# Kernel optimization log

Measured on AMD Instinct MI355X. Metric: run time of the kernel, lower is better.

The kernel has to match this reference:

```python
import jax, jax.numpy as jnp
from jax import lax
import numpy as np

EPS = 0.15      # constraint_value_upper_bound (per-row box |y/c - 1| <= EPS)
DELTA = 0.05    # groups_constraint_upper_bound (per-group mean |y/c - 1| <= DELTA)
N_GROUPS = 8
N_ITERS = 300   # Dykstra iterations; converges to the exact QP projection

N, D, H1, H2, K = 65536, 512, 1024, 512, 1


def setup_inputs() -> dict:
    key = jax.random.key(0)
    ks = jax.random.split(key, 8)
    x = jax.random.normal(ks[0], (N, D), jnp.float32)
    W1 = jax.random.normal(ks[1], (D, H1), jnp.float32) / np.float32(np.sqrt(D))
    b1 = jnp.zeros((H1,), jnp.float32)
    W2 = jax.random.normal(ks[2], (H1, H2), jnp.float32) / np.float32(np.sqrt(H1))
    b2 = jnp.zeros((H2,), jnp.float32)
    Wf = jax.random.normal(ks[3], (H2, K), jnp.float32) / np.float32(np.sqrt(H2))
    bf = jnp.zeros((K,), jnp.float32)
    c = jax.random.uniform(ks[4], (N,), jnp.float32, 0.5, 2.0)
    # quantiles_price_tensor: q_i = (1/N) * #{k : c_k <= c_i}  (rank via searchsorted)
    q = jnp.searchsorted(jnp.sort(c), c, side='right').astype(jnp.float32) / N
    # group j covers q in [j/G, (j+1)/G]; assign boundary ties to the lower group
    g = jnp.clip(jnp.ceil(q * N_GROUPS).astype(jnp.int32) - 1, 0, N_GROUPS - 1)
    group_mask = jax.nn.one_hot(g, N_GROUPS, dtype=jnp.float32).T  # [G, N]
    return dict(x=x, W1=W1, b1=b1, W2=W2, b2=b2, Wf=Wf, bf=bf,
                constraint_constant=c, group_mask=group_mask)


def _project(y_u, c, group_mask):
    """Exact QP: min ||y - y_u||^2 s.t. |y_i/c_i - 1| <= EPS and
    |mean_{i in G_j}(y_i/c_i - 1)| <= DELTA, solved by Dykstra's alternating
    projections in z = y/c - 1 space under the weighted norm sum c_i^2 z_i^2."""
    w = c * c                                   # [N] weights of the norm
    z0 = y_u / c[:, None] - 1.0                 # [N, K]
    n = group_mask.sum(axis=1)                  # [G] group sizes
    a = group_mask / n[:, None]                 # [G, N] averaging rows
    denom = (a * a / w[None, :]).sum(axis=1)    # [G]  a^T W^{-1} a
    u = (a / w[None, :]) / denom[:, None]       # [G, N] weighted slab directions

    def proj_box(z):
        return jnp.clip(z, -EPS, EPS)

    def proj_grp(z):
        v = a @ z                               # [G, K] group means
        return z - u.T @ (v - jnp.clip(v, -DELTA, DELTA))

    def body(carry, _):
        z, p, q = carry
        zb = proj_box(z + p); p = z + p - zb
        zg = proj_grp(zb + q); q = zb + q - zg
        return (zg, p, q), None

    init = (z0, jnp.zeros_like(z0), jnp.zeros_like(z0))
    (z, _, _), _ = lax.scan(body, init, None, length=N_ITERS)
    return (z + 1.0) * c[:, None]


def reference(x, W1, b1, W2, b2, Wf, bf, constraint_constant, group_mask):
    h = jax.nn.relu(x @ W1 + b1)   # Dropout is identity in eval mode
    h = jax.nn.relu(h @ W2 + b2)
    y_u = h @ Wf + bf              # [N, 1] unconstrained predictions
    return _project(y_u, constraint_constant, group_mask)
```

## Files before the change

### kernel.cpp

```cpp
#include <hip/hip_runtime.h>
#include <hip/hip_bf16.h>

#define NROWS 65536
#define DIM   512
#define H1DIM 1024
#define H2DIM 512
#define EPSC  0.15f
#define DELTA 0.05f
#define NGRP  8
#define CAPG  16384

typedef __bf16 bf16x8 __attribute__((ext_vector_type(8)));
typedef float  f32x4  __attribute__((ext_vector_type(4)));

__device__ __forceinline__ void gload16(const void* g, void* lds) {
  __builtin_amdgcn_global_load_lds((__attribute__((address_space(1))) const unsigned int*)g,
                                   (__attribute__((address_space(3))) unsigned int*)lds,
                                   16, 0, 0);
}

__global__ void k_zero(float* y_u, int n, int* cnt) {
  int i = blockIdx.x * blockDim.x + threadIdx.x;
  if (i < n) y_u[i] = 0.f;
  if (i < NGRP) cnt[i] = 0;
}

__global__ void k_tcvt(const float* __restrict__ src, __bf16* __restrict__ dst, int R, int C) {
  __shared__ float tile[32][33];
  const int bi = blockIdx.x * 32;
  const int bj = blockIdx.y * 32;
  const int tx = threadIdx.x, ty = threadIdx.y;
  #pragma unroll
  for (int r = ty; r < 32; r += 8)
    tile[r][tx] = src[(size_t)(bi + r) * C + bj + tx];
  __syncthreads();
  #pragma unroll
  for (int r = ty; r < 32; r += 8)
    dst[(size_t)(bj + r) * R + bi + tx] = (__bf16)tile[tx][r];
}

__global__ __launch_bounds__(512, 2) void k_gemm1(const float* __restrict__ x,
                                                  const __bf16* __restrict__ w1t,
                                                  const float* __restrict__ b1,
                                                  __bf16* __restrict__ h1, int row0) {
  __shared__ __align__(16) __bf16 As[2][256 * 64];
  __shared__ __align__(16) __bf16 Bs[2][256 * 64];
  const int tid = threadIdx.x;
  const int w = tid >> 6, l = tid & 63;
  const int mt   = (int)gridDim.x >> 2;
  const int mper = mt >> 3;
  const int xcd  = blockIdx.x & 7;
  const int idx  = blockIdx.x >> 3;
  const int brow = (xcd * mper + (idx >> 2)) * 256;
  const int bcol = (idx & 3) * 256;
  const int lr = l & 15, lk = l >> 4;
  const int wm = w >> 2, wn = w & 3;
  const int mbase = wm * 128, nbase = wn * 64;
  const int srow = w * 32 + (l >> 3);
  const int scol = (l & 7) * 8;
  const int NT = DIM / 64;
  f32x4 acc[8][4] = {};
  const float* xp = x + (size_t)(row0 + brow + srow) * DIM + scol;

  #define LOADA(KT, F) do { \
    _Pragma("unroll") for (int t_ = 0; t_ < 4; ++t_) { \
      const float* s_ = xp + (size_t)(t_ * 8) * DIM + (KT); \
      F[t_][0] = *(const float4*)s_; F[t_][1] = *(const float4*)(s_ + 4); } } while (0)
  #define STOREB(KT, BUF) do { \
    _Pragma("unroll") for (int t_ = 0; t_ < 4; ++t_) \
      gload16(w1t + (size_t)(bcol + srow + t_ * 8) * DIM + (KT) + scol, \
              Bs[BUF] + (w * 32 + t_ * 8) * 64); } while (0)
  #define CVTA(BUF, F) do { \
    _Pragma("unroll") for (int t_ = 0; t_ < 4; ++t_) { \
      bf16x8 v_; \
      v_[0] = (__bf16)F[t_][0].x; v_[1] = (__bf16)F[t_][0].y; \
      v_[2] = (__bf16)F[t_][0].z; v_[3] = (__bf16)F[t_][0].w; \
      v_[4] = (__bf16)F[t_][1].x; v_[5] = (__bf16)F[t_][1].y; \
      v_[6] = (__bf16)F[t_][1].z; v_[7] = (__bf16)F[t_][1].w; \
      *(bf16x8*)(As[BUF] + (w * 32 + t_ * 8) * 64 + (l >> 3) * 64 + scol) = v_; } } while (0)
  #define COMPUTE(BUF) do { \
    _Pragma("unroll") for (int kk = 0; kk < 64; kk += 32) { \
      bf16x8 af[8], bq[4]; \
      _Pragma("unroll") for (int m = 0; m < 8; ++m) \
        af[m] = *(const bf16x8*)(As[BUF] + (mbase + m * 16 + lr) * 64 + kk + lk * 8); \
      _Pragma("unroll") for (int nn = 0; nn < 4; ++nn) \
        bq[nn] = *(const bf16x8*)(Bs[BUF] + (nbase + nn * 16 + lr) * 64 + kk + lk * 8); \
      __builtin_amdgcn_s_setprio(1); \
      _Pragma("unroll") for (int m = 0; m < 8; ++m) \
        _Pragma("unroll") for (int nn = 0; nn < 4; ++nn) \
          acc[m][nn] = __builtin_amdgcn_mfma_f32_16x16x32_bf16(af[m], bq[nn], acc[m][nn], 0, 0, 0); \
      __builtin_amdgcn_s_setprio(0); \
    } } while (0)

  {
    float4 f[4][2];
    LOADA(0, f);
    STOREB(0, 0);
    CVTA(0, f);
  }
  __syncthreads();
  int cur = 0;
  for (int t = 0; t < NT - 1; ++t) {
    const int ktn = (t + 1) * 64;
    float4 f[4][2];
    LOADA(ktn, f);
    STOREB(ktn, cur ^ 1);
    COMPUTE(cur);
    CVTA(cur ^ 1, f);
    __syncthreads();
    cur ^= 1;
  }
  COMPUTE(cur);

  #undef LOADA
  #undef STOREB
  #undef CVTA
  #undef COMPUTE

  #pragma unroll
  for (int nn = 0; nn < 4; ++nn) {
    const int col = bcol + nbase + nn * 16 + lr;
    const float bias = b1[col];
    #pragma unroll
    for (int m = 0; m < 8; ++m) {
      const int row = brow + mbase + m * 16 + lk * 4;
      #pragma unroll
      for (int j = 0; j < 4; ++j) {
        float v = acc[m][nn][j] + bias;
        v = fmaxf(v, 0.f);
        h1[(size_t)(row + j) * H1DIM + col] = (__bf16)v;
      }
    }
  }
}

__global__ __launch_bounds__(512, 2) void k_gemm2(const __bf16* __restrict__ h1,
                                                  const __bf16* __restrict__ w2t,
                                                  const float* __restrict__ b2,
                                                  const float* __restrict__ wf,
                                                  float* __restrict__ y_u, int row0) {
  __shared__ __align__(16) __bf16 As[2][256 * 64];
  __shared__ __align__(16) __bf16 Bs[2][256 * 64];
  __shared__ float yred[256];
  const int tid = threadIdx.x;
  const int w = tid >> 6, l = tid & 63;
  const int mt   = (int)gridDim.x >> 1;
  const int mper = mt >> 3;
  const int xcd  = blockIdx.x & 7;
  const int idx  = blockIdx.x >> 3;
  const int brow = (xcd * mper + (idx >> 1)) * 256;
  const int n0   = (idx & 1) * 256;
  const int lr = l & 15, lk = l >> 4;
  const int wm = w >> 2, wn = w & 3;
  const int mbase = wm * 128, nbase = wn * 64;
  const int srow = w * 32 + (l >> 3);
  const int scol = (l & 7) * 8;
  const int NT = H1DIM / 64;
  f32x4 acc[8][4] = {};

  #define STAGE2(KT, BUF) do { \
    _Pragma("unroll") for (int t_ = 0; t_ < 4; ++t_) { \
      gload16(h1  + (size_t)(brow + srow + t_ * 8) * H1DIM + (KT) + scol, \
              As[BUF] + (w * 32 + t_ * 8) * 64); \
      gload16(w2t + (size_t)(n0   + srow + t_ * 8) * H1DIM + (KT) + scol, \
              Bs[BUF] + (w * 32 + t_ * 8) * 64); } } while (0)
  #define COMPUTE2(BUF) do { \
    _Pragma("unroll") for (int kk = 0; kk < 64; kk += 32) { \
      bf16x8 af[8], bq[4]; \
      _Pragma("unroll") for (int m = 0; m < 8; ++m) \
        af[m] = *(const bf16x8*)(As[BUF] + (mbase + m * 16 + lr) * 64 + kk + lk * 8); \
      _Pragma("unroll") for (int nn = 0; nn < 4; ++nn) \
        bq[nn] = *(const bf16x8*)(Bs[BUF] + (nbase + nn * 16 + lr) * 64 + kk + lk * 8); \
      __builtin_amdgcn_s_setprio(1); \
      _Pragma("unroll") for (int m = 0; m < 8; ++m) \
        _Pragma("unroll") for (int nn = 0; nn < 4; ++nn) \
          acc[m][nn] = __builtin_amdgcn_mfma_f32_16x16x32_bf16(af[m], bq[nn], acc[m][nn], 0, 0, 0); \
      __builtin_amdgcn_s_setprio(0); \
    } } while (0)

  STAGE2(0, 0);
  __syncthreads();
  int cur = 0;
  for (int t = 0; t < NT - 1; ++t) {
    STAGE2((t + 1) * 64, cur ^ 1);
    COMPUTE2(cur);
    __syncthreads();
    cur ^= 1;
  }
  COMPUTE2(cur);

  #undef STAGE2
  #undef COMPUTE2

  float yacc[8][4] = {};
  #pragma unroll
  for (int nn = 0; nn < 4; ++nn) {
    const int col = n0 + nbase + nn * 16 + lr;
    const float bias = b2[col];
    const float wfv = wf[col];
    #pragma unroll
    for (int m = 0; m < 8; ++m)
      #pragma unroll
      for (int j = 0; j < 4; ++j)
        yacc[m][j] += fmaxf(acc[m][nn][j] + bias, 0.f) * wfv;
  }
  #pragma unroll
  for (int m = 0; m < 8; ++m)
    #pragma unroll
    for (int j = 0; j < 4; ++j) {
      float v = yacc[m][j];
      v += __shfl_xor(v, 1, 64);
      v += __shfl_xor(v, 2, 64);
      v += __shfl_xor(v, 4, 64);
      v += __shfl_xor(v, 8, 64);
      yacc[m][j] = v;
    }
  if (tid < 256) yred[tid] = 0.f;
  __syncthreads();
  if (lr == 0) {
    #pragma unroll
    for (int m = 0; m < 8; ++m)
      #pragma unroll
      for (int j = 0; j < 4; ++j)
        atomicAdd(&yred[mbase + m * 16 + lk * 4 + j], yacc[m][j]);
  }
  __syncthreads();
  if (tid < 256) atomicAdd(&y_u[row0 + brow + tid], yred[tid]);
}

__global__ __launch_bounds__(256) void k_scatter(const float* __restrict__ y_u,
                                                 const float* __restrict__ c,
                                                 const float* __restrict__ mask,
                                                 const float* __restrict__ bfp,
                                                 float* __restrict__ z0c, float* __restrict__ wc,
                                                 unsigned char* __restrict__ gidx,
                                                 int* __restrict__ cnt, int n) {
  __shared__ int lcnt[NGRP];
  __shared__ int lbase[NGRP];
  const float bf0 = bfp[0];
  const int tid = threadIdx.x;
  if (tid < NGRP) lcnt[tid] = 0;
  __syncthreads();
  const int i = blockIdx.x * blockDim.x + tid;
  int g = 0, slot_l = 0;
  float z0 = 0.f, wv = 0.f;
  if (i < n) {
    const float cv = c[i];
    z0 = (y_u[i] + bf0) / cv - 1.f;
    wv = cv * cv;
    #pragma unroll
    for (int j = 1; j < NGRP; ++j)
      if (mask[(size_t)j * NROWS + i] > 0.5f) g = j;
    slot_l = atomicAdd(&lcnt[g], 1);
    gidx[i] = (unsigned char)g;
  }
  __syncthreads();
  if (tid < NGRP) lbase[tid] = atomicAdd(&cnt[tid], lcnt[tid]);
  __syncthreads();
  if (i < n) {
    const int slot = lbase[g] + slot_l;
    if (slot < CAPG) {
      z0c[(size_t)g * CAPG + slot] = z0;
      wc [(size_t)g * CAPG + slot] = wv;
    }
  }
}

__device__ __forceinline__ float wave_red(float v, int mode) {
  #pragma unroll
  for (int o = 32; o > 0; o >>= 1) {
    float u = __shfl_xor(v, o, 64);
    v = (mode == 0) ? (v + u) : ((mode == 1) ? fmaxf(v, u) : fminf(v, u));
  }
  return v;
}
__device__ __forceinline__ float block_red(float v, int mode, float* red, int tid) {
  v = wave_red(v, mode);
  if ((tid & 63) == 0) red[tid >> 6] = v;
  __syncthreads();
  if (tid < 64) {
    float x = (tid < 16) ? red[tid] : (mode == 0 ? 0.f : (mode == 1 ? -1e30f : 1e30f));
    x = wave_red(x, mode);
    if (tid == 0) red[0] = x;
  }
  __syncthreads();
  float r = red[0];
  __syncthreads();
  return r;
}

__global__ __launch_bounds__(1024) void k_mu(const float* __restrict__ z0c,
                                             const float* __restrict__ wc,
                                             const int* __restrict__ cnt,
                                             float* __restrict__ muarr) {
  __shared__ float red[16];
  const int g = blockIdx.x;
  const int tid = threadIdx.x;
  int n = cnt[g];
  if (n > CAPG) n = CAPG;
  if (n <= 0) { if (tid == 0) muarr[g] = 0.f; return; }
  float z0v[16], iwv[16];
  float hmax = -1e30f, hmin = 1e30f;
  #pragma unroll
  for (int t = 0; t < 16; ++t) {
    const int idx = t * 1024 + tid;
    if (idx < n) {
      const float z0 = z0c[(size_t)g * CAPG + idx];
      const float wv = wc[(size_t)g * CAPG + idx];
      z0v[t] = z0; iwv[t] = 1.f / wv;
      hmax = fmaxf(hmax, (z0 + EPSC) * wv);
      hmin = fminf(hmin, (z0 - EPSC) * wv);
    } else { z0v[t] = 0.f; iwv[t] = 0.f; }
  }
  const float inv_n = 1.f / (float)n;
  #define EVALM(MU, OUT) do { float s_ = 0.f; \
    _Pragma("unroll") for (int t = 0; t < 16; ++t) \
      s_ += fminf(fmaxf(z0v[t] - (MU) * iwv[t], -EPSC), EPSC); \
    OUT = block_red(s_, 0, red, tid) * inv_n; } while (0)
  float m0; EVALM(0.f, m0);
  float mu = 0.f;
  if (fabsf(m0) > DELTA) {
    float target, lo, hi;
    if (m0 > 0.f) { target = DELTA;  lo = 0.f; hi = block_red(hmax, 1, red, tid); }
    else          { target = -DELTA; hi = 0.f; lo = block_red(hmin, 2, red, tid); }
    for (int it = 0; it < 40; ++it) {
      const float mid = 0.5f * (lo + hi);
      float mm; EVALM(mid, mm);
      if (mm >= target) lo = mid; else hi = mid;
    }
    mu = 0.5f * (lo + hi);
  }
  if (tid == 0) muarr[g] = mu;
  #undef EVALM
}

__global__ void k_y(const float* __restrict__ y_u, const float* __restrict__ c,
                    const float* __restrict__ bfp, const unsigned char* __restrict__ gidx,
                    const float* __restrict__ muarr, float* __restrict__ out, int n) {
  const float bf0 = bfp[0];
  int i = blockIdx.x * blockDim.x + threadIdx.x;
  const int stride = gridDim.x * blockDim.x;
  for (; i < n; i += stride) {
    const float cv = c[i];
    const float z0 = (y_u[i] + bf0) / cv - 1.f;
    const float wv = cv * cv;
    const float mu = muarr[gidx[i]];
    const float z = fminf(fmaxf(z0 - mu / wv, -EPSC), EPSC);
    out[i] = (z + 1.f) * cv;
  }
}

extern "C" void kernel_launch(void* const* d_in, const int* in_sizes, int n_in,
                              void* d_out, int out_size, void* d_ws, size_t ws_size,
                              hipStream_t stream) {
  const float* x    = (const float*)d_in[0];
  const float* W1   = (const float*)d_in[1];
  const float* b1   = (const float*)d_in[2];
  const float* W2   = (const float*)d_in[3];
  const float* b2   = (const float*)d_in[4];
  const float* Wf   = (const float*)d_in[5];
  const float* bfp  = (const float*)d_in[6];
  const float* c    = (const float*)d_in[7];
  const float* mask = (const float*)d_in[8];
  float* out = (float*)d_out;

  char* ws = (char*)d_ws;
  size_t off = 0;
  auto alloc = [&](size_t bytes) -> void* {
    void* p = ws + off;
    off += (bytes + 255) & ~(size_t)255;
    return p;
  };
  __bf16* w1t = (__bf16*)alloc((size_t)H1DIM * DIM * 2);
  __bf16* w2t = (__bf16*)alloc((size_t)H2DIM * H1DIM * 2);
  float* y_u  = (float*)alloc((size_t)NROWS * 4);
  float* z0c  = (float*)alloc((size_t)NGRP * CAPG * 4);
  float* wc   = (float*)alloc((size_t)NGRP * CAPG * 4);
  unsigned char* gidx = (unsigned char*)alloc(NROWS);
  int*   cnt  = (int*)alloc(NGRP * 4);
  float* muarr = (float*)alloc(NGRP * 4);
  const size_t fixed = off;

  size_t avail = (ws_size > fixed) ? (ws_size - fixed) : 0;
  long long rc = (long long)(avail / ((size_t)H1DIM * 2));
  rc &= ~2047LL;
  if (rc > 32768) rc = 32768;
  if (rc < 2048) rc = 2048;
  const int rows_chunk = (int)rc;
  __bf16* h1 = (__bf16*)(ws + fixed);

  k_zero<<<dim3((NROWS + 255) / 256), dim3(256), 0, stream>>>(y_u, NROWS, cnt);
  k_tcvt<<<dim3(DIM / 32, H1DIM / 32), dim3(32, 8), 0, stream>>>(W1, w1t, DIM, H1DIM);
  k_tcvt<<<dim3(H1DIM / 32, H2DIM / 32), dim3(32, 8), 0, stream>>>(W2, w2t, H1DIM, H2DIM);

  for (int r0 = 0; r0 < NROWS; r0 += rows_chunk) {
    const int Mc = (NROWS - r0 < rows_chunk) ? (NROWS - r0) : rows_chunk;
    const int mtiles = Mc / 256;
    k_gemm1<<<dim3(mtiles * 4), dim3(512), 0, stream>>>(x, w1t, b1, h1, r0);
    k_gemm2<<<dim3(mtiles * 2), dim3(512), 0, stream>>>(h1, w2t, b2, Wf, y_u, r0);
  }

  k_scatter<<<dim3((NROWS + 255) / 256), dim3(256), 0, stream>>>(y_u, c, mask, bfp, z0c, wc, gidx, cnt, NROWS);
  k_mu<<<dim3(NGRP), dim3(1024), 0, stream>>>(z0c, wc, cnt, muarr);
  k_y<<<dim3(256), dim3(256), 0, stream>>>(y_u, c, bfp, gidx, muarr, out, NROWS);
}
```

Measured before the change: 262.9 us.

## Pre-convert x to bf16 in a separate pass and stream A via LDS-direct loads

Result: slower. 273.5 us (+4.1%).

```diff
diff --git a/kernel.cpp b/kernel.cpp
--- a/kernel.cpp
+++ b/kernel.cpp
@@ -39,10 +39,24 @@
     dst[(size_t)(bj + r) * R + bi + tx] = (__bf16)tile[tx][r];
 }
 
-__global__ __launch_bounds__(512, 2) void k_gemm1(const float* __restrict__ x,
+__global__ __launch_bounds__(256) void k_cvt_x(const float4* __restrict__ x4,
+                                               bf16x8* __restrict__ xb8, int n8) {
+  int i = blockIdx.x * blockDim.x + threadIdx.x;
+  const int stride = gridDim.x * blockDim.x;
+  for (; i < n8; i += stride) {
+    const float4 a = x4[2 * i];
+    const float4 b = x4[2 * i + 1];
+    bf16x8 v;
+    v[0] = (__bf16)a.x; v[1] = (__bf16)a.y; v[2] = (__bf16)a.z; v[3] = (__bf16)a.w;
+    v[4] = (__bf16)b.x; v[5] = (__bf16)b.y; v[6] = (__bf16)b.z; v[7] = (__bf16)b.w;
+    xb8[i] = v;
+  }
+}
+
+__global__ __launch_bounds__(512, 2) void k_gemm1(const __bf16* __restrict__ xb,
                                                   const __bf16* __restrict__ w1t,
                                                   const float* __restrict__ b1,
-                                                  __bf16* __restrict__ h1, int row0) {
+                                                  __bf16* __restrict__ h1) {
   __shared__ __align__(16) __bf16 As[2][256 * 64];
   __shared__ __align__(16) __bf16 Bs[2][256 * 64];
   const int tid = threadIdx.x;
@@ -60,25 +74,14 @@
   const int scol = (l & 7) * 8;
   const int NT = DIM / 64;
   f32x4 acc[8][4] = {};
-  const float* xp = x + (size_t)(row0 + brow + srow) * DIM + scol;
-
-  #define LOADA(KT, F) do { \
+
+  #define STAGE1(KT, BUF) do { \
     _Pragma("unroll") for (int t_ = 0; t_ < 4; ++t_) { \
-      const float* s_ = xp + (size_t)(t_ * 8) * DIM + (KT); \
-      F[t_][0] = *(const float4*)s_; F[t_][1] = *(const float4*)(s_ + 4); } } while (0)
-  #define STOREB(KT, BUF) do { \
-    _Pragma("unroll") for (int t_ = 0; t_ < 4; ++t_) \
+      gload16(xb  + (size_t)(brow + srow + t_ * 8) * DIM + (KT) + scol, \
+              As[BUF] + (w * 32 + t_ * 8) * 64); \
       gload16(w1t + (size_t)(bcol + srow + t_ * 8) * DIM + (KT) + scol, \
-              Bs[BUF] + (w * 32 + t_ * 8) * 64); } while (0)
-  #define CVTA(BUF, F) do { \
-    _Pragma("unroll") for (int t_ = 0; t_ < 4; ++t_) { \
-      bf16x8 v_; \
-      v_[0] = (__bf16)F[t_][0].x; v_[1] = (__bf16)F[t_][0].y; \
-      v_[2] = (__bf16)F[t_][0].z; v_[3] = (__bf16)F[t_][0].w; \
-      v_[4] = (__bf16)F[t_][1].x; v_[5] = (__bf16)F[t_][1].y; \
-      v_[6] = (__bf16)F[t_][1].z; v_[7] = (__bf16)F[t_][1].w; \
-      *(bf16x8*)(As[BUF] + (w * 32 + t_ * 8) * 64 + (l >> 3) * 64 + scol) = v_; } } while (0)
-  #define COMPUTE(BUF) do { \
+              Bs[BUF] + (w * 32 + t_ * 8) * 64); } } while (0)
+  #define COMPUTE1(BUF) do { \
     _Pragma("unroll") for (int kk = 0; kk < 64; kk += 32) { \
       bf16x8 af[8], bq[4]; \
       _Pragma("unroll") for (int m = 0; m < 8; ++m) \
@@ -92,30 +95,19 @@
       __builtin_amdgcn_s_setprio(0); \
     } } while (0)
 
-  {
-    float4 f[4][2];
-    LOADA(0, f);
-    STOREB(0, 0);
-    CVTA(0, f);
-  }
+  STAGE1(0, 0);
   __syncthreads();
   int cur = 0;
   for (int t = 0; t < NT - 1; ++t) {
-    const int ktn = (t + 1) * 64;
-    float4 f[4][2];
-    LOADA(ktn, f);
-    STOREB(ktn, cur ^ 1);
-    COMPUTE(cur);
-    CVTA(cur ^ 1, f);
+    STAGE1((t + 1) * 64, cur ^ 1);
+    COMPUTE1(cur);
     __syncthreads();
     cur ^= 1;
   }
-  COMPUTE(cur);
-
-  #undef LOADA
-  #undef STOREB
-  #undef CVTA
-  #undef COMPUTE
+  COMPUTE1(cur);
+
+  #undef STAGE1
+  #undef COMPUTE1
 
   #pragma unroll
   for (int nn = 0; nn < 4; ++nn) {
@@ -323,7 +315,7 @@
     float target, lo, hi;
     if (m0 > 0.f) { target = DELTA;  lo = 0.f; hi = block_red(hmax, 1, red, tid); }
     else          { target = -DELTA; hi = 0.f; lo = block_red(hmin, 2, red, tid); }
-    for (int it = 0; it < 40; ++it) {
+    for (int it = 0; it < 32; ++it) {
       const float mid = 0.5f * (lo + hi);
       float mm; EVALM(mid, mm);
       if (mm >= target) lo = mid; else hi = mid;
@@ -382,12 +374,13 @@
   const size_t fixed = off;
 
   size_t avail = (ws_size > fixed) ? (ws_size - fixed) : 0;
-  long long rc = (long long)(avail / ((size_t)H1DIM * 2));
+  long long rc = (long long)(avail / ((size_t)(DIM + H1DIM * 2)));
   rc &= ~2047LL;
   if (rc > 32768) rc = 32768;
   if (rc < 2048) rc = 2048;
   const int rows_chunk = (int)rc;
-  __bf16* h1 = (__bf16*)(ws + fixed);
+  __bf16* xb = (__bf16*)(ws + fixed);
+  __bf16* h1 = (__bf16*)(ws + fixed + (size_t)rows_chunk * DIM * 2);
 
   k_zero<<<dim3((NROWS + 255) / 256), dim3(256), 0, stream>>>(y_u, NROWS, cnt);
   k_tcvt<<<dim3(DIM / 32, H1DIM / 32), dim3(32, 8), 0, stream>>>(W1, w1t, DIM, H1DIM);
@@ -396,7 +389,11 @@
   for (int r0 = 0; r0 < NROWS; r0 += rows_chunk) {
     const int Mc = (NROWS - r0 < rows_chunk) ? (NROWS - r0) : rows_chunk;
     const int mtiles = Mc / 256;
-    k_gemm1<<<dim3(mtiles * 4), dim3(512), 0, stream>>>(x, w1t, b1, h1, r0);
+    const int n8 = Mc * (DIM / 8);
+    int cblocks = (n8 + 255) / 256; if (cblocks > 2048) cblocks = 2048;
+    k_cvt_x<<<dim3(cblocks), dim3(256), 0, stream>>>(
+        (const float4*)(x + (size_t)r0 * DIM), (bf16x8*)xb, n8);
+    k_gemm1<<<dim3(mtiles * 4), dim3(512), 0, stream>>>(xb, w1t, b1, h1);
     k_gemm2<<<dim3(mtiles * 2), dim3(512), 0, stream>>>(h1, w2t, b2, Wf, y_u, r0);
   }
 
```
